# Kernel tuning notes

Hardware: AMD Instinct MI355X
Metric: run time of the kernel (lower is better)

Reference implementation:

```python
import jax, jax.numpy as jnp
import numpy as np

N_NODES = 50000
N_EDGES = 600000
D_FEAT = 128
NHID = 128
N_CLASSES = 40


def gcn_conv(x, W, b, src, dst, n_nodes):
    """PyG-style GCNConv: out = D^{-1/2} (A + I) D^{-1/2} (x W) + b.

    src/dst: [E'] edge endpoints including self-loops; messages are gathered
    from src and scatter-added at dst with symmetric normalization.
    """
    h = x @ W  # [N, out] -- transform before propagate (linearity => same math)
    deg = jax.ops.segment_sum(jnp.ones_like(dst, dtype=h.dtype), dst,
                              num_segments=n_nodes)  # in-degree incl. self-loop
    dinv = jnp.where(deg > 0, jax.lax.rsqrt(deg), 0.0)
    norm = dinv[src] * dinv[dst]  # [E']
    msg = h[src] * norm[:, None]  # [E', out] gather + scale
    out = jax.ops.segment_sum(msg, dst, num_segments=n_nodes)  # scatter-add
    return out + b


def setup_inputs() -> dict:
    key = jax.random.key(0)
    ks = jax.random.split(key, 8)
    x = jax.random.normal(ks[0], (N_NODES, D_FEAT), dtype=jnp.float32)
    edge_index = jax.random.randint(ks[1], (2, N_EDGES), 0, N_NODES, dtype=jnp.int64)
    # Glorot-ish scaled params
    W1 = jax.random.normal(ks[2], (D_FEAT, NHID), dtype=jnp.float32) / np.sqrt(D_FEAT)
    b1 = jnp.zeros((NHID,), dtype=jnp.float32)
    W2 = jax.random.normal(ks[3], (NHID, NHID), dtype=jnp.float32) / np.sqrt(NHID)
    b2 = jnp.zeros((NHID,), dtype=jnp.float32)
    Wlin = jax.random.normal(ks[4], (NHID, N_CLASSES), dtype=jnp.float32) / np.sqrt(NHID)
    blin = jnp.zeros((N_CLASSES,), dtype=jnp.float32)
    return {"x": x, "edge_index": edge_index, "W1": W1, "b1": b1,
            "W2": W2, "b2": b2, "Wlin": Wlin, "blin": blin}


def reference(x, edge_index, W1, b1, W2, b2, Wlin, blin):
    n = x.shape[0]
    loop = jnp.arange(n, dtype=edge_index.dtype)
    src = jnp.concatenate([edge_index[0], loop])  # add self-loops
    dst = jnp.concatenate([edge_index[1], loop])
    h = gcn_conv(x, W1, b1, src, dst, n)
    h = jnp.tanh(h)  # dropout is identity in eval mode
    h = gcn_conv(h, W2, b2, src, dst, n)
    h = jnp.tanh(h)
    return h @ Wlin + blin  # [N, num_classes]
```

## Files before the change

kernel.cpp:

```cpp
#include <hip/hip_runtime.h>
#include <cmath>

#define D 128
#define NCLS 40
#define GG 391
#define CAP 64

typedef __bf16 bfrag __attribute__((ext_vector_type(8)));
typedef float ffrag __attribute__((ext_vector_type(4)));
typedef unsigned int u32;
typedef unsigned int u32x4 __attribute__((ext_vector_type(4)));

__global__ __launch_bounds__(256) void mega1(const float* __restrict__ A, const float* __restrict__ W1,
                                             const float* __restrict__ W2, const float* __restrict__ Wl,
                                             __bf16* __restrict__ C, int N,
                                             const int* __restrict__ src, const int* __restrict__ dst, int E,
                                             int* __restrict__ deg, int* __restrict__ csr,
                                             __bf16* __restrict__ Wt2, __bf16* __restrict__ Wlt, int EB) {
  const int b = blockIdx.x;
  const int tid = threadIdx.x;
  if (b >= GG) {
    if (b < GG + EB) {
      int e = (b - GG) * 256 + tid;
      if (e < E) {
        int s = src[e], d = dst[e];
        int pos = atomicAdd(&deg[d], 1);
        if (pos < CAP) csr[d * CAP + pos] = s;
      }
    } else {
      int j = (b - GG - EB) * 256 + tid;
      if (j < 16384) {
        Wt2[j] = (__bf16)W2[(j & 127) * D + (j >> 7)];
      } else if (j < 16384 + 48 * D) {
        int q = j - 16384;
        int n = q >> 7, k = q & 127;
        Wlt[q] = (n < NCLS) ? (__bf16)Wl[k * NCLS + n] : (__bf16)0.0f;
      }
    }
    return;
  }
  __shared__ __align__(16) __bf16 Bs[128][136];
  const int wave = tid >> 6, lane = tid & 63;
  const int row0 = b * 128 + wave * 32;
  const int koff = (lane >> 4) * 8;

  for (int i = tid; i < 128 * 128; i += 256) {
    int n = i & 127, k = i >> 7;
    Bs[n][k] = (__bf16)W1[k * D + n];
  }

  bfrag a[2][4];
#pragma unroll
  for (int mt = 0; mt < 2; ++mt) {
    int r = row0 + mt * 16 + (lane & 15);
    int rc = r < N ? r : N - 1;
    const float* p = A + (size_t)rc * D;
#pragma unroll
    for (int kk = 0; kk < 4; ++kk) {
      float4 u = *(const float4*)(p + kk * 32 + koff);
      float4 v = *(const float4*)(p + kk * 32 + koff + 4);
      bfrag f;
      f[0] = (__bf16)u.x; f[1] = (__bf16)u.y; f[2] = (__bf16)u.z; f[3] = (__bf16)u.w;
      f[4] = (__bf16)v.x; f[5] = (__bf16)v.y; f[6] = (__bf16)v.z; f[7] = (__bf16)v.w;
      a[mt][kk] = f;
    }
  }
  __syncthreads();

  ffrag acc[2][8];
#pragma unroll
  for (int mt = 0; mt < 2; ++mt)
#pragma unroll
    for (int n = 0; n < 8; ++n) acc[mt][n] = (ffrag){0.f, 0.f, 0.f, 0.f};

#pragma unroll
  for (int kk = 0; kk < 4; ++kk) {
#pragma unroll
    for (int n = 0; n < 8; ++n) {
      bfrag bb = *(const bfrag*)(&Bs[n * 16 + (lane & 15)][kk * 32 + koff]);
      acc[0][n] = __builtin_amdgcn_mfma_f32_16x16x32_bf16(a[0][kk], bb, acc[0][n], 0, 0, 0);
      acc[1][n] = __builtin_amdgcn_mfma_f32_16x16x32_bf16(a[1][kk], bb, acc[1][n], 0, 0, 0);
    }
  }

  int ocol = lane & 15;
#pragma unroll
  for (int mt = 0; mt < 2; ++mt) {
    int orow0 = row0 + mt * 16 + (lane >> 4) * 4;
#pragma unroll
    for (int n = 0; n < 8; ++n)
#pragma unroll
      for (int i = 0; i < 4; ++i) {
        int r = orow0 + i;
        if (r < N) C[(size_t)r * D + n * 16 + ocol] = (__bf16)acc[mt][n][i];
      }
  }
}

__global__ __launch_bounds__(256) void gather_bf16(const __bf16* __restrict__ t, const int* __restrict__ deg,
                                                   const int* __restrict__ csr, const float* __restrict__ bias,
                                                   __bf16* __restrict__ out, int N) {
  int node = blockIdx.x * 4 + (threadIdx.x >> 6);
  if (node >= N) return;
  const int lane = threadIdx.x & 63;
  const int g = lane >> 4, sl = lane & 15;
  const int cnt = __builtin_amdgcn_readfirstlane(deg[node]);
  const int jmax = cnt < CAP ? cnt : CAP;
  const float dv = rsqrtf((float)cnt + 1.0f);
  const int beg = node * CAP;

  int es = 0;
  float ew = 0.0f;
  if (lane < jmax) {
    es = csr[beg + lane];
    ew = rsqrtf((float)deg[es] + 1.0f) * dv;
  }

  bfrag tv = *(const bfrag*)(t + (size_t)node * D + sl * 8);
  float selfw = (g == 0) ? dv * dv : 0.0f;
  float acc[8];
#pragma unroll
  for (int i = 0; i < 8; ++i) acc[i] = selfw * (float)tv[i];

  for (int j = 0; j < jmax; j += 4) {
    int idx = j + g;
    int c = idx < jmax ? idx : jmax - 1;
    int s = __shfl(es, c, 64);
    float wv = __shfl(ew, c, 64);
    float w = idx < jmax ? wv : 0.0f;
    bfrag r = *(const bfrag*)(t + (size_t)s * D + sl * 8);
#pragma unroll
    for (int i = 0; i < 8; ++i) acc[i] += w * (float)r[i];
  }

#pragma unroll
  for (int i = 0; i < 8; ++i) {
    acc[i] += __shfl_xor(acc[i], 16, 64);
    acc[i] += __shfl_xor(acc[i], 32, 64);
  }

  if (g == 0) {
    float4 b0 = *(const float4*)(bias + sl * 8);
    float4 b1 = *(const float4*)(bias + sl * 8 + 4);
    bfrag o;
    o[0] = (__bf16)tanhf(acc[0] + b0.x);
    o[1] = (__bf16)tanhf(acc[1] + b0.y);
    o[2] = (__bf16)tanhf(acc[2] + b0.z);
    o[3] = (__bf16)tanhf(acc[3] + b0.w);
    o[4] = (__bf16)tanhf(acc[4] + b1.x);
    o[5] = (__bf16)tanhf(acc[5] + b1.y);
    o[6] = (__bf16)tanhf(acc[6] + b1.z);
    o[7] = (__bf16)tanhf(acc[7] + b1.w);
    __builtin_nontemporal_store(*(u32x4*)&o, (u32x4*)(out + (size_t)node * D + sl * 8));
  }
}

__global__ __launch_bounds__(256) void gemm_mfma(const __bf16* __restrict__ A, const __bf16* __restrict__ Wt,
                                                 __bf16* __restrict__ C, int N) {
  __shared__ __align__(16) __bf16 Bs[128][136];
  const int tid = threadIdx.x;
  const int wave = tid >> 6, lane = tid & 63;
  const int row0 = blockIdx.x * 128 + wave * 32;
  const int koff = (lane >> 4) * 8;

  for (int i = tid; i < 128 * 16; i += 256) {
    int n = i >> 4, seg = i & 15;
    *(uint4*)&Bs[n][seg * 8] = *(const uint4*)(Wt + n * D + seg * 8);
  }

  bfrag a[2][4];
#pragma unroll
  for (int mt = 0; mt < 2; ++mt) {
    int r = row0 + mt * 16 + (lane & 15);
    int rc = r < N ? r : N - 1;
#pragma unroll
    for (int kk = 0; kk < 4; ++kk)
      a[mt][kk] = *(const bfrag*)(A + (size_t)rc * D + kk * 32 + koff);
  }
  __syncthreads();

  ffrag acc[2][8];
#pragma unroll
  for (int mt = 0; mt < 2; ++mt)
#pragma unroll
    for (int n = 0; n < 8; ++n) acc[mt][n] = (ffrag){0.f, 0.f, 0.f, 0.f};

#pragma unroll
  for (int kk = 0; kk < 4; ++kk) {
#pragma unroll
    for (int n = 0; n < 8; ++n) {
      bfrag b = *(const bfrag*)(&Bs[n * 16 + (lane & 15)][kk * 32 + koff]);
      acc[0][n] = __builtin_amdgcn_mfma_f32_16x16x32_bf16(a[0][kk], b, acc[0][n], 0, 0, 0);
      acc[1][n] = __builtin_amdgcn_mfma_f32_16x16x32_bf16(a[1][kk], b, acc[1][n], 0, 0, 0);
    }
  }

  int ocol = lane & 15;
#pragma unroll
  for (int mt = 0; mt < 2; ++mt) {
    int orow0 = row0 + mt * 16 + (lane >> 4) * 4;
#pragma unroll
    for (int n = 0; n < 8; ++n)
#pragma unroll
      for (int i = 0; i < 4; ++i) {
        int r = orow0 + i;
        if (r < N) C[(size_t)r * D + n * 16 + ocol] = (__bf16)acc[mt][n][i];
      }
  }
}

__global__ __launch_bounds__(256) void head_mfma(const __bf16* __restrict__ H, const __bf16* __restrict__ Wlt,
                                                 const float* __restrict__ bias, float* __restrict__ out, int N) {
  __shared__ __align__(16) __bf16 Ws[48][136];
  const int tid = threadIdx.x;
  const int wave = tid >> 6, lane = tid & 63;
  const int row0 = blockIdx.x * 128 + wave * 32;
  const int koff = (lane >> 4) * 8;

  for (int i = tid; i < 48 * 16; i += 256) {
    int n = i >> 4, seg = i & 15;
    *(uint4*)&Ws[n][seg * 8] = *(const uint4*)(Wlt + n * D + seg * 8);
  }

  bfrag a[2][4];
#pragma unroll
  for (int mt = 0; mt < 2; ++mt) {
    int r = row0 + mt * 16 + (lane & 15);
    int rc = r < N ? r : N - 1;
#pragma unroll
    for (int kk = 0; kk < 4; ++kk)
      a[mt][kk] = *(const bfrag*)(H + (size_t)rc * D + kk * 32 + koff);
  }
  __syncthreads();

  ffrag acc[2][3];
#pragma unroll
  for (int mt = 0; mt < 2; ++mt)
#pragma unroll
    for (int n = 0; n < 3; ++n) acc[mt][n] = (ffrag){0.f, 0.f, 0.f, 0.f};

#pragma unroll
  for (int kk = 0; kk < 4; ++kk) {
#pragma unroll
    for (int n = 0; n < 3; ++n) {
      bfrag b = *(const bfrag*)(&Ws[n * 16 + (lane & 15)][kk * 32 + koff]);
      acc[0][n] = __builtin_amdgcn_mfma_f32_16x16x32_bf16(a[0][kk], b, acc[0][n], 0, 0, 0);
      acc[1][n] = __builtin_amdgcn_mfma_f32_16x16x32_bf16(a[1][kk], b, acc[1][n], 0, 0, 0);
    }
  }

  int ocol = lane & 15;
#pragma unroll
  for (int mt = 0; mt < 2; ++mt) {
    int orow0 = row0 + mt * 16 + (lane >> 4) * 4;
#pragma unroll
    for (int n = 0; n < 3; ++n) {
      int c = n * 16 + ocol;
      if (c < NCLS) {
#pragma unroll
        for (int i = 0; i < 4; ++i) {
          int r = orow0 + i;
          if (r < N) out[(size_t)r * NCLS + c] = acc[mt][n][i] + bias[c];
        }
      }
    }
  }
}

extern "C" void kernel_launch(void* const* d_in, const int* in_sizes, int n_in,
                              void* d_out, int out_size, void* d_ws, size_t ws_size,
                              hipStream_t stream) {
  const float* x    = (const float*)d_in[0];
  const int*   ei   = (const int*)d_in[1];
  const float* W1   = (const float*)d_in[2];
  const float* b1   = (const float*)d_in[3];
  const float* W2   = (const float*)d_in[4];
  const float* b2   = (const float*)d_in[5];
  const float* Wlin = (const float*)d_in[6];
  const float* blin = (const float*)d_in[7];
  float* out = (float*)d_out;

  const int N = in_sizes[0] / D;
  const int E = in_sizes[1] / 2;
  const int* srcp = ei;
  const int* dstp = ei + E;

  char* ws = (char*)d_ws;
  int*    deg = (int*)ws;
  __bf16* Wt2 = (__bf16*)(ws + ((size_t)256 << 10));
  __bf16* Wlt = (__bf16*)(ws + ((size_t)320 << 10));
  int*    csr = (int*)(ws + ((size_t)1 << 20));
  __bf16* tb  = (__bf16*)(ws + ((size_t)16 << 20));
  __bf16* hb  = (__bf16*)(ws + ((size_t)32 << 20));

  const int eb = (E + 255) / 256;
  const int cvb = (16384 + 48 * D + 255) / 256;
  dim3 b256(256);

  (void)hipMemsetAsync(deg, 0, (size_t)N * sizeof(int), stream);
  mega1<<<GG + eb + cvb, b256, 0, stream>>>(x, W1, W2, Wlin, tb, N, srcp, dstp, E, deg, csr, Wt2, Wlt, eb);
  gather_bf16<<<(N + 3) / 4, b256, 0, stream>>>(tb, deg, csr, b1, hb, N);
  gemm_mfma<<<GG, b256, 0, stream>>>(hb, Wt2, tb, N);
  gather_bf16<<<(N + 3) / 4, b256, 0, stream>>>(tb, deg, csr, b2, hb, N);
  head_mfma<<<GG, b256, 0, stream>>>(hb, Wlt, blin, out, N);
}
```

Measured before the change: 205.5 us.

## Fuse neighbor gather with following GEMM and head via shared-memory tiles

Each block now gathers and aggregates 16 nodes, applies bias and tanh, and stages the bf16 rows in shared memory. It then runs the next dense transform (W2, or the final linear head) with MFMA straight from that tile. This removes two kernel launches and the global round trip of the intermediate hidden activations. The memset is also replaced by a small zeroing kernel. In exchange, every block reloads its weight fragments from global/L2 memory, and each wave handles four nodes serially, which may reduce latency hiding in the gather.

```diff
diff --git a/kernel.cpp b/kernel.cpp
--- a/kernel.cpp
+++ b/kernel.cpp
@@ -10,6 +10,11 @@
 typedef float ffrag __attribute__((ext_vector_type(4)));
 typedef unsigned int u32;
 typedef unsigned int u32x4 __attribute__((ext_vector_type(4)));
+
+__global__ __launch_bounds__(256) void zero_deg(int* __restrict__ deg, int N) {
+  int i = blockIdx.x * 256 + threadIdx.x;
+  if (i < N) deg[i] = 0;
+}
 
 __global__ __launch_bounds__(256) void mega1(const float* __restrict__ A, const float* __restrict__ W1,
                                              const float* __restrict__ W2, const float* __restrict__ Wl,
@@ -97,28 +102,21 @@
   }
 }
 
-__global__ __launch_bounds__(256) void gather_bf16(const __bf16* __restrict__ t, const int* __restrict__ deg,
-                                                   const int* __restrict__ csr, const float* __restrict__ bias,
-                                                   __bf16* __restrict__ out, int N) {
-  int node = blockIdx.x * 4 + (threadIdx.x >> 6);
-  if (node >= N) return;
-  const int lane = threadIdx.x & 63;
-  const int g = lane >> 4, sl = lane & 15;
+__device__ inline void gather_node(const __bf16* __restrict__ t, const int* __restrict__ deg,
+                                   const int* __restrict__ csr, int node, int lane, int g, int sl,
+                                   float acc[8]) {
   const int cnt = __builtin_amdgcn_readfirstlane(deg[node]);
   const int jmax = cnt < CAP ? cnt : CAP;
   const float dv = rsqrtf((float)cnt + 1.0f);
   const int beg = node * CAP;
-
   int es = 0;
   float ew = 0.0f;
   if (lane < jmax) {
     es = csr[beg + lane];
     ew = rsqrtf((float)deg[es] + 1.0f) * dv;
   }
-
   bfrag tv = *(const bfrag*)(t + (size_t)node * D + sl * 8);
   float selfw = (g == 0) ? dv * dv : 0.0f;
-  float acc[8];
 #pragma unroll
   for (int i = 0; i < 8; ++i) acc[i] = selfw * (float)tv[i];
 
@@ -132,136 +130,129 @@
 #pragma unroll
     for (int i = 0; i < 8; ++i) acc[i] += w * (float)r[i];
   }
-
 #pragma unroll
   for (int i = 0; i < 8; ++i) {
     acc[i] += __shfl_xor(acc[i], 16, 64);
     acc[i] += __shfl_xor(acc[i], 32, 64);
   }
-
-  if (g == 0) {
-    float4 b0 = *(const float4*)(bias + sl * 8);
-    float4 b1 = *(const float4*)(bias + sl * 8 + 4);
-    bfrag o;
-    o[0] = (__bf16)tanhf(acc[0] + b0.x);
-    o[1] = (__bf16)tanhf(acc[1] + b0.y);
-    o[2] = (__bf16)tanhf(acc[2] + b0.z);
-    o[3] = (__bf16)tanhf(acc[3] + b0.w);
-    o[4] = (__bf16)tanhf(acc[4] + b1.x);
-    o[5] = (__bf16)tanhf(acc[5] + b1.y);
-    o[6] = (__bf16)tanhf(acc[6] + b1.z);
-    o[7] = (__bf16)tanhf(acc[7] + b1.w);
-    __builtin_nontemporal_store(*(u32x4*)&o, (u32x4*)(out + (size_t)node * D + sl * 8));
-  }
-}
-
-__global__ __launch_bounds__(256) void gemm_mfma(const __bf16* __restrict__ A, const __bf16* __restrict__ Wt,
-                                                 __bf16* __restrict__ C, int N) {
-  __shared__ __align__(16) __bf16 Bs[128][136];
+}
+
+__global__ __launch_bounds__(256) void gather_gemm(const __bf16* __restrict__ t, const int* __restrict__ deg,
+                                                   const int* __restrict__ csr, const float* __restrict__ bias,
+                                                   const __bf16* __restrict__ Wt, __bf16* __restrict__ C, int N) {
+  __shared__ __align__(16) __bf16 Hs[16][136];
   const int tid = threadIdx.x;
   const int wave = tid >> 6, lane = tid & 63;
-  const int row0 = blockIdx.x * 128 + wave * 32;
-  const int koff = (lane >> 4) * 8;
-
-  for (int i = tid; i < 128 * 16; i += 256) {
-    int n = i >> 4, seg = i & 15;
-    *(uint4*)&Bs[n][seg * 8] = *(const uint4*)(Wt + n * D + seg * 8);
-  }
-
-  bfrag a[2][4];
-#pragma unroll
-  for (int mt = 0; mt < 2; ++mt) {
-    int r = row0 + mt * 16 + (lane & 15);
-    int rc = r < N ? r : N - 1;
+  const int g = lane >> 4, sl = lane & 15;
+  const int node0 = blockIdx.x * 16;
+
+#pragma unroll 1
+  for (int m = 0; m < 4; ++m) {
+    int node = node0 + wave * 4 + m;
+    if (node < N) {
+      float acc[8];
+      gather_node(t, deg, csr, node, lane, g, sl, acc);
+      if (g == 0) {
+        float4 b0 = *(const float4*)(bias + sl * 8);
+        float4 b1 = *(const float4*)(bias + sl * 8 + 4);
+        bfrag o;
+        o[0] = (__bf16)tanhf(acc[0] + b0.x);
+        o[1] = (__bf16)tanhf(acc[1] + b0.y);
+        o[2] = (__bf16)tanhf(acc[2] + b0.z);
+        o[3] = (__bf16)tanhf(acc[3] + b0.w);
+        o[4] = (__bf16)tanhf(acc[4] + b1.x);
+        o[5] = (__bf16)tanhf(acc[5] + b1.y);
+        o[6] = (__bf16)tanhf(acc[6] + b1.z);
+        o[7] = (__bf16)tanhf(acc[7] + b1.w);
+        *(u32x4*)&Hs[wave * 4 + m][sl * 8] = *(u32x4*)&o;
+      }
+    }
+  }
+  __syncthreads();
+
+  const int koff = g * 8;
+  bfrag a[4];
+#pragma unroll
+  for (int kk = 0; kk < 4; ++kk) a[kk] = *(const bfrag*)(&Hs[sl][kk * 32 + koff]);
+  ffrag acc2[2];
+  acc2[0] = (ffrag){0.f, 0.f, 0.f, 0.f};
+  acc2[1] = (ffrag){0.f, 0.f, 0.f, 0.f};
+#pragma unroll
+  for (int nt = 0; nt < 2; ++nt) {
+    const __bf16* wp = Wt + (size_t)(wave * 32 + nt * 16 + sl) * D;
+    bfrag bfr[4];
+#pragma unroll
+    for (int kk = 0; kk < 4; ++kk) bfr[kk] = *(const bfrag*)(wp + kk * 32 + koff);
 #pragma unroll
     for (int kk = 0; kk < 4; ++kk)
-      a[mt][kk] = *(const bfrag*)(A + (size_t)rc * D + kk * 32 + koff);
-  }
-  __syncthreads();
-
-  ffrag acc[2][8];
-#pragma unroll
-  for (int mt = 0; mt < 2; ++mt)
-#pragma unroll
-    for (int n = 0; n < 8; ++n) acc[mt][n] = (ffrag){0.f, 0.f, 0.f, 0.f};
-
-#pragma unroll
-  for (int kk = 0; kk < 4; ++kk) {
-#pragma unroll
-    for (int n = 0; n < 8; ++n) {
-      bfrag b = *(const bfrag*)(&Bs[n * 16 + (lane & 15)][kk * 32 + koff]);
-      acc[0][n] = __builtin_amdgcn_mfma_f32_16x16x32_bf16(a[0][kk], b, acc[0][n], 0, 0, 0);
-      acc[1][n] = __builtin_amdgcn_mfma_f32_16x16x32_bf16(a[1][kk], b, acc[1][n], 0, 0, 0);
-    }
-  }
-
-  int ocol = lane & 15;
-#pragma unroll
-  for (int mt = 0; mt < 2; ++mt) {
-    int orow0 = row0 + mt * 16 + (lane >> 4) * 4;
-#pragma unroll
-    for (int n = 0; n < 8; ++n)
-#pragma unroll
-      for (int i = 0; i < 4; ++i) {
-        int r = orow0 + i;
-        if (r < N) C[(size_t)r * D + n * 16 + ocol] = (__bf16)acc[mt][n][i];
-      }
-  }
-}
-
-__global__ __launch_bounds__(256) void head_mfma(const __bf16* __restrict__ H, const __bf16* __restrict__ Wlt,
-                                                 const float* __restrict__ bias, float* __restrict__ out, int N) {
-  __shared__ __align__(16) __bf16 Ws[48][136];
+      acc2[nt] = __builtin_amdgcn_mfma_f32_16x16x32_bf16(a[kk], bfr[kk], acc2[nt], 0, 0, 0);
+  }
+#pragma unroll
+  for (int nt = 0; nt < 2; ++nt) {
+    int ccol = wave * 32 + nt * 16 + sl;
+#pragma unroll
+    for (int i = 0; i < 4; ++i) {
+      int r = node0 + g * 4 + i;
+      if (r < N) C[(size_t)r * D + ccol] = (__bf16)acc2[nt][i];
+    }
+  }
+}
+
+__global__ __launch_bounds__(256) void gather_head(const __bf16* __restrict__ t, const int* __restrict__ deg,
+                                                   const int* __restrict__ csr, const float* __restrict__ bias,
+                                                   const __bf16* __restrict__ Wlt, const float* __restrict__ blin,
+                                                   float* __restrict__ out, int N) {
+  __shared__ __align__(16) __bf16 Hs[16][136];
   const int tid = threadIdx.x;
   const int wave = tid >> 6, lane = tid & 63;
-  const int row0 = blockIdx.x * 128 + wave * 32;
-  const int koff = (lane >> 4) * 8;
-
-  for (int i = tid; i < 48 * 16; i += 256) {
-    int n = i >> 4, seg = i & 15;
-    *(uint4*)&Ws[n][seg * 8] = *(const uint4*)(Wlt + n * D + seg * 8);
-  }
-
-  bfrag a[2][4];
-#pragma unroll
-  for (int mt = 0; mt < 2; ++mt) {
-    int r = row0 + mt * 16 + (lane & 15);
-    int rc = r < N ? r : N - 1;
+  const int g = lane >> 4, sl = lane & 15;
+  const int node0 = blockIdx.x * 16;
+
+#pragma unroll 1
+  for (int m = 0; m < 4; ++m) {
+    int node = node0 + wave * 4 + m;
+    if (node < N) {
+      float acc[8];
+      gather_node(t, deg, csr, node, lane, g, sl, acc);
+      if (g == 0) {
+        float4 b0 = *(const float4*)(bias + sl * 8);
+        float4 b1 = *(const float4*)(bias + sl * 8 + 4);
+        bfrag o;
+        o[0] = (__bf16)tanhf(acc[0] + b0.x);
+        o[1] = (__bf16)tanhf(acc[1] + b0.y);
+        o[2] = (__bf16)tanhf(acc[2] + b0.z);
+        o[3] = (__bf16)tanhf(acc[3] + b0.w);
+        o[4] = (__bf16)tanhf(acc[4] + b1.x);
+        o[5] = (__bf16)tanhf(acc[5] + b1.y);
+        o[6] = (__bf16)tanhf(acc[6] + b1.z);
+        o[7] = (__bf16)tanhf(acc[7] + b1.w);
+        *(u32x4*)&Hs[wave * 4 + m][sl * 8] = *(u32x4*)&o;
+      }
+    }
+  }
+  __syncthreads();
+
+  if (wave < 3) {
+    const int koff = g * 8;
+    bfrag a[4];
+#pragma unroll
+    for (int kk = 0; kk < 4; ++kk) a[kk] = *(const bfrag*)(&Hs[sl][kk * 32 + koff]);
+    ffrag acc2 = (ffrag){0.f, 0.f, 0.f, 0.f};
+    const __bf16* wp = Wlt + (size_t)(wave * 16 + sl) * D;
+    bfrag bfr[4];
+#pragma unroll
+    for (int kk = 0; kk < 4; ++kk) bfr[kk] = *(const bfrag*)(wp + kk * 32 + koff);
 #pragma unroll
     for (int kk = 0; kk < 4; ++kk)
-      a[mt][kk] = *(const bfrag*)(H + (size_t)rc * D + kk * 32 + koff);
-  }
-  __syncthreads();
-
-  ffrag acc[2][3];
-#pragma unroll
-  for (int mt = 0; mt < 2; ++mt)
-#pragma unroll
-    for (int n = 0; n < 3; ++n) acc[mt][n] = (ffrag){0.f, 0.f, 0.f, 0.f};
-
-#pragma unroll
-  for (int kk = 0; kk < 4; ++kk) {
-#pragma unroll
-    for (int n = 0; n < 3; ++n) {
-      bfrag b = *(const bfrag*)(&Ws[n * 16 + (lane & 15)][kk * 32 + koff]);
-      acc[0][n] = __builtin_amdgcn_mfma_f32_16x16x32_bf16(a[0][kk], b, acc[0][n], 0, 0, 0);
-      acc[1][n] = __builtin_amdgcn_mfma_f32_16x16x32_bf16(a[1][kk], b, acc[1][n], 0, 0, 0);
-    }
-  }
-
-  int ocol = lane & 15;
-#pragma unroll
-  for (int mt = 0; mt < 2; ++mt) {
-    int orow0 = row0 + mt * 16 + (lane >> 4) * 4;
-#pragma unroll
-    for (int n = 0; n < 3; ++n) {
-      int c = n * 16 + ocol;
-      if (c < NCLS) {
-#pragma unroll
-        for (int i = 0; i < 4; ++i) {
-          int r = orow0 + i;
-          if (r < N) out[(size_t)r * NCLS + c] = acc[mt][n][i] + bias[c];
-        }
+      acc2 = __builtin_amdgcn_mfma_f32_16x16x32_bf16(a[kk], bfr[kk], acc2, 0, 0, 0);
+
+    int ccol = wave * 16 + sl;
+    if (ccol < NCLS) {
+      float bl = blin[ccol];
+#pragma unroll
+      for (int i = 0; i < 4; ++i) {
+        int r = node0 + g * 4 + i;
+        if (r < N) out[(size_t)r * NCLS + ccol] = acc2[i] + bl;
       }
     }
   }
@@ -293,14 +284,14 @@
   __bf16* tb  = (__bf16*)(ws + ((size_t)16 << 20));
   __bf16* hb  = (__bf16*)(ws + ((size_t)32 << 20));
 
+  const int nb = (N + 255) / 256;
   const int eb = (E + 255) / 256;
   const int cvb = (16384 + 48 * D + 255) / 256;
+  const int gb = (N + 15) / 16;
   dim3 b256(256);
 
-  (void)hipMemsetAsync(deg, 0, (size_t)N * sizeof(int), stream);
+  zero_deg<<<nb, b256, 0, stream>>>(deg, N);
   mega1<<<GG + eb + cvb, b256, 0, stream>>>(x, W1, W2, Wlin, tb, N, srcp, dstp, E, deg, csr, Wt2, Wlt, eb);
-  gather_bf16<<<(N + 3) / 4, b256, 0, stream>>>(tb, deg, csr, b1, hb, N);
-  gemm_mfma<<<GG, b256, 0, stream>>>(hb, Wt2, tb, N);
-  gather_bf16<<<(N + 3) / 4, b256, 0, stream>>>(tb, deg, csr, b2, hb, N);
-  head_mfma<<<GG, b256, 0, stream>>>(hb, Wlt, blin, out, N);
-}
+  gather_gemm<<<gb, b256, 0, stream>>>(tb, deg, csr, b1, Wt2, hb, N);
+  gather_head<<<gb, b256, 0, stream>>>(hb, deg, csr, b2, Wlt, blin, out, N);
+}
```

Result: no change. 203.7 us (-0.9%).
